# Performance work log

Measured on AMD Instinct MI355X. Metric: run time of the kernel, lower is better.

The kernel has to match this reference:

```python
import jax, jax.numpy as jnp
import numpy as np

N, M_CHE, M_VDW, B = 20000, 20, 20, 200
H, E, NODE_IN, NCONV = 128, 20, 13, 3
CHE_CUTOFF, VDW_CUTOFF = 8.0, 12.0


def setup_inputs() -> dict:
    key = jax.random.key(0)
    ks = jax.random.split(key, 16)
    s = 0.05
    inp = {}
    inp['atoms_embed'] = jax.random.normal(ks[0], (N, NODE_IN), jnp.float32)
    inp['che_nbrs_fea'] = jax.random.uniform(ks[1], (N, M_CHE), jnp.float32, 0.5, CHE_CUTOFF * 1.1)
    inp['vdw_nbrs_fea'] = jax.random.uniform(ks[2], (N, M_VDW), jnp.float32, 0.5, VDW_CUTOFF * 1.1)
    inp['che_nbrs_idx'] = jax.random.randint(ks[3], (N, M_CHE), 0, N)
    inp['vdw_nbrs_idx'] = jax.random.randint(ks[4], (N, M_VDW), 0, N)
    inp['num_atoms'] = jnp.full((B,), N // B, dtype=jnp.int32)  # 200 crystals x 100 atoms
    inp['emb_W'] = jax.random.normal(ks[5], (NODE_IN, H), jnp.float32) * s
    inp['emb_b'] = jnp.zeros((H,), jnp.float32)
    inp['che_filter_W'] = jax.random.normal(ks[6], (NCONV, E, H), jnp.float32) * s
    inp['che_filter_b'] = jnp.zeros((NCONV, H), jnp.float32)
    inp['che_fc_W'] = jax.random.normal(ks[7], (NCONV, 3 * H, 2 * H), jnp.float32) * s
    inp['che_fc_b'] = jnp.zeros((NCONV, 2 * H), jnp.float32)
    inp['vdw_filter_W'] = jax.random.normal(ks[8], (NCONV, E, H), jnp.float32) * s
    inp['vdw_filter_b'] = jnp.zeros((NCONV, H), jnp.float32)
    inp['vdw_fc_W'] = jax.random.normal(ks[9], (NCONV, 3 * H, 2 * H), jnp.float32) * s
    inp['vdw_fc_b'] = jnp.zeros((NCONV, 2 * H), jnp.float32)
    inp['fc1_W'] = jax.random.normal(ks[10], (H, H), jnp.float32) * s
    inp['fc1_b'] = jnp.zeros((H,), jnp.float32)
    inp['out_W'] = jax.random.normal(ks[11], (H, 1), jnp.float32) * s
    inp['out_b'] = jnp.zeros((1,), jnp.float32)
    return inp


def _rbf(d, cutoff):
    # sinc-like radial basis with cosine envelope; zero beyond cutoff
    k = jnp.arange(1, E + 1, dtype=d.dtype)  # [E]
    de = d[..., None]  # [N, M, 1]
    r = jnp.where(de < cutoff, jnp.sin(de * k * (jnp.pi / cutoff)) / de, jnp.zeros((), d.dtype))
    env = 0.5 * (jnp.cos(jnp.pi * d / cutoff) + 1.0)
    return r * env[..., None]  # [N, M, E]


def _conv_half(nodes, rbf_e, idx, fW, fb, gW, gb):
    n, m = idx.shape
    edges = rbf_e @ fW + fb  # [N, M, H]
    self_fea = jnp.broadcast_to(nodes[:, None, :], (n, m, nodes.shape[1]))
    total = jnp.concatenate([self_fea, edges, nodes[idx]], axis=2)  # [N, M, 3H]
    gated = total @ gW + gb  # [N, M, 2H]
    filt, core = jnp.split(gated, 2, axis=2)
    return jnp.sum(jax.nn.sigmoid(filt) * jax.nn.softplus(core), axis=1)  # [N, H]


def reference(atoms_embed, che_nbrs_fea, che_nbrs_idx, vdw_nbrs_fea, vdw_nbrs_idx,
              num_atoms, emb_W, emb_b, che_filter_W, che_filter_b, che_fc_W, che_fc_b,
              vdw_filter_W, vdw_filter_b, vdw_fc_W, vdw_fc_b, fc1_W, fc1_b, out_W, out_b):
    nodes = atoms_embed @ emb_W + emb_b  # [N, H]
    che_rbf = _rbf(che_nbrs_fea, CHE_CUTOFF)
    vdw_rbf = _rbf(vdw_nbrs_fea, VDW_CUTOFF)
    for i in range(NCONV):
        che = _conv_half(nodes, che_rbf, che_nbrs_idx, che_filter_W[i], che_filter_b[i], che_fc_W[i], che_fc_b[i])
        vdw = _conv_half(nodes, vdw_rbf, vdw_nbrs_idx, vdw_filter_W[i], vdw_filter_b[i], vdw_fc_W[i], vdw_fc_b[i])
        nodes = jax.nn.softplus(nodes + che + vdw)
    # per-crystal mean pooling from contiguous atom ranges given by num_atoms
    ends = jnp.cumsum(num_atoms)
    seg = jnp.searchsorted(ends, jnp.arange(nodes.shape[0]), side='right')
    sums = jax.ops.segment_sum(nodes, seg, num_segments=B)
    crys = sums / num_atoms[:, None].astype(nodes.dtype)  # [B, H]
    crys = jax.nn.softplus(jax.nn.softplus(crys) @ fc1_W + fc1_b)
    predict = (crys @ out_W + out_b)[:, 0]  # [B]
    return predict
```

## Files before the change

kernel.cpp:

```cpp
#include <hip/hip_runtime.h>
#include <hip/hip_bf16.h>
#include <math.h>

#define NN 20000
#define MM 20
#define EE 20
#define HH 128
#define BB 200
#define NCONV 3
#define CHE_CUT 8.0f
#define VDW_CUT 12.0f
#define PI_F 3.14159265358979323846f
#define LOG2E_F 1.44269504088896340736f
#define LN2_F 0.69314718055994530942f

typedef __fp16 half2_t __attribute__((ext_vector_type(2)));
typedef _Float16 f16x8 __attribute__((ext_vector_type(8)));
typedef float f32x4 __attribute__((ext_vector_type(4)));

__device__ __forceinline__ float exp2_(float x) {
#if __has_builtin(__builtin_amdgcn_exp2f)
    return __builtin_amdgcn_exp2f(x);
#else
    return exp2f(x);
#endif
}
__device__ __forceinline__ float log2_(float x) {
#if __has_builtin(__builtin_amdgcn_logf)
    return __builtin_amdgcn_logf(x);
#else
    return log2f(x);
#endif
}
__device__ __forceinline__ float rcp_(float x) {
#if __has_builtin(__builtin_amdgcn_rcpf)
    return __builtin_amdgcn_rcpf(x);
#else
    return 1.f / x;
#endif
}
__device__ __forceinline__ float sp_(float x) {
    return (x > 15.f) ? x : LN2_F * log2_(1.f + exp2_(x * LOG2E_F));
}
__device__ __forceinline__ float fdot2_(half2_t a, half2_t b, float c) {
#if __has_builtin(__builtin_amdgcn_fdot2)
    return __builtin_amdgcn_fdot2(a, b, c, false);
#else
    return (float)a.x * (float)b.x + (float)a.y * (float)b.y + c;
#endif
}

__global__ void prep_bias(const float* __restrict__ cfb, const float* __restrict__ cgW,
                          const float* __restrict__ cgb,
                          const float* __restrict__ vfb, const float* __restrict__ vgW,
                          const float* __restrict__ vgb, float* __restrict__ bc) {
    int half = blockIdx.y;
    int l = blockIdx.z;
    int j = threadIdx.x;
    const float* fb = half ? vfb : cfb;
    const float* gW = half ? vgW : cgW;
    const float* gb = half ? vgb : cgb;
    const float* gWe = gW + ((size_t)l * 384 + 128) * 256;
    const float* brow = fb + (size_t)l * HH;
    float acc = gb[(size_t)l * 256 + j];
    for (int k = 0; k < HH; ++k) acc = fmaf(brow[k], gWe[k * 256 + j], acc);
    bc[((size_t)l * 2 + half) * 256 + j] = acc * LOG2E_F;
}

__global__ void prep_bwc(const float* __restrict__ cfW, const float* __restrict__ cgW,
                         const float* __restrict__ vfW, const float* __restrict__ vgW,
                         _Float16* __restrict__ bwc) {
    int nt = blockIdx.x;
    int half = blockIdx.y;
    int l = blockIdx.z;
    int tid = threadIdx.x;
    int k = tid >> 4, nc = tid & 15;
    int t = (nt & 7) * 16 + nc;
    int gcol = (nt >> 3) * 128 + t;
    const float* fW = half ? vfW : cfW;
    const float* gW = half ? vgW : cgW;
    const float* gWe = gW + ((size_t)l * 384 + 128) * 256;
    float val = 0.f;
    if (k < EE) {
        const float* frow = fW + ((size_t)l * EE + k) * HH;
        for (int kk = 0; kk < HH; ++kk) val = fmaf(frow[kk], gWe[kk * 256 + gcol], val);
        val *= LOG2E_F;
    }
    bwc[(((size_t)(l * 2 + half) * 16 + nt) * 64 + (k >> 3) * 16 + nc) * 8 + (k & 7)] = (_Float16)val;
}

__global__ void prep_bpk(const float* __restrict__ cgW, const float* __restrict__ vgW,
                         _Float16* __restrict__ bpk) {
    int i = blockIdx.x * 256 + threadIdx.x;
    if (i >= NCONV * 128 * 1024) return;
    int l = i >> 17;
    int rem = i & 131071;
    int k = rem >> 10;
    int c = rem & 1023;
    int half = (c >> 8) & 1;
    const float* src = half ? vgW : cgW;
    int grow = l * 384 + ((c < 512) ? k : 256 + k);
    float val = src[(size_t)grow * 256 + (c & 255)] * LOG2E_F;
    int nt = c >> 4, nc = c & 15;
    int s = k >> 5, kq = (k >> 3) & 3, j = k & 7;
    bpk[(size_t)l * 131072 + (((size_t)nt * 4 + s) * 64 + kq * 16 + nc) * 8 + j] = (_Float16)val;
}

__global__ void embed_kernel(const float* __restrict__ atoms, const float* __restrict__ W,
                             const float* __restrict__ bias, float* __restrict__ nodes,
                             _Float16* __restrict__ nodes_h) {
    int n = blockIdx.x, t = threadIdx.x;
    const float* arow = atoms + (size_t)n * 13;
    float acc = bias[t];
    #pragma unroll
    for (int k = 0; k < 13; ++k) acc = fmaf(arow[k], W[k * HH + t], acc);
    nodes[(size_t)n * HH + t] = acc;
    nodes_h[(size_t)n * HH + t] = (_Float16)acc;
}

__global__ void rbf_kernel(const float* __restrict__ che_fea, const float* __restrict__ vdw_fea,
                           _Float16* __restrict__ rfrag) {
    int i = blockIdx.x * blockDim.x + threadIdx.x;
    if (i >= 2 * NN * MM) return;
    bool isv = i >= NN * MM;
    int rem = isv ? i - NN * MM : i;
    int n = rem / MM, m = rem % MM;
    float d = isv ? vdw_fea[rem] : che_fea[rem];
    float cutoff = isv ? VDW_CUT : CHE_CUT;
    float x = d * (PI_F / cutoff);
    float s1 = sinf(x), c1 = cosf(x);
    float env = 0.5f * (c1 + 1.f);
    float scale = (d < cutoff) ? (env / d) : 0.f;
    float out[EE];
    float skm1 = 0.f, sk = s1;
    #pragma unroll
    for (int e = 0; e < EE; ++e) {
        out[e] = sk * scale;
        float nx = 2.f * c1 * sk - skm1;
        skm1 = sk; sk = nx;
    }
    int mt = m >> 4, la = m & 15;
    _Float16* base = rfrag + (((size_t)(isv ? NN + n : n) * 2 + mt) * 64) * 8 + la * 8;
    f16x8 v0, v1, v2, v3;
    #pragma unroll
    for (int j = 0; j < 8; ++j) {
        v0[j] = (_Float16)out[j];
        v1[j] = (_Float16)out[8 + j];
        v2[j] = (j < 4) ? (_Float16)out[16 + j] : (_Float16)0.f;
        v3[j] = (_Float16)0.f;
    }
    *(f16x8*)(base) = v0;
    *(f16x8*)(base + 128) = v1;
    *(f16x8*)(base + 256) = v2;
    *(f16x8*)(base + 384) = v3;
}

__global__ __launch_bounds__(256)
void gemm_mfma(const _Float16* __restrict__ Ah, const _Float16* __restrict__ Bpk,
               half2_t* __restrict__ Spk, half2_t* __restrict__ Ypk) {
    int lane = threadIdx.x & 63;
    int wv = threadIdx.x >> 6;
    int m0 = blockIdx.x * 16;
    int la = lane & 15;
    int quad = lane >> 4;
    int k0 = quad * 8;

    f16x8 af[4];
    {
        const _Float16* arow = Ah + (size_t)(m0 + la) * 128 + k0;
        #pragma unroll
        for (int s = 0; s < 4; ++s)
            af[s] = *(const f16x8*)(arow + s * 32);
    }

    const f16x8* bp = (const f16x8*)Bpk;
    int ntf0 = wv * 16;
    half2_t* dst = (wv & 2) ? Ypk : Spk;
    int wbase = (wv & 1) * 128 + la;

    f16x8 fb[4], cb[4], nfb[4], ncb[4];
    #pragma unroll
    for (int s = 0; s < 4; ++s) {
        fb[s] = bp[((size_t)ntf0 * 4 + s) * 64 + lane];
        cb[s] = bp[((size_t)(ntf0 + 8) * 4 + s) * 64 + lane];
    }
    for (int p = 0; p < 8; ++p) {
        if (p < 7) {
            #pragma unroll
            for (int s = 0; s < 4; ++s) {
                nfb[s] = bp[((size_t)(ntf0 + p + 1) * 4 + s) * 64 + lane];
                ncb[s] = bp[((size_t)(ntf0 + 9 + p) * 4 + s) * 64 + lane];
            }
        }
        f32x4 accf = {0.f, 0.f, 0.f, 0.f};
        f32x4 accc = {0.f, 0.f, 0.f, 0.f};
        #pragma unroll
        for (int s = 0; s < 4; ++s) {
            accf = __builtin_amdgcn_mfma_f32_16x16x32_f16(af[s], fb[s], accf, 0, 0, 0);
            accc = __builtin_amdgcn_mfma_f32_16x16x32_f16(af[s], cb[s], accc, 0, 0, 0);
        }
        int row = m0 + quad * 4;
        int word = wbase + p * 16;
        #pragma unroll
        for (int i = 0; i < 4; ++i) {
            half2_t pk = __builtin_amdgcn_cvt_pkrtz(accf[i], accc[i]);
            dst[(size_t)(row + i) * 256 + word] = pk;
        }
        #pragma unroll
        for (int s = 0; s < 4; ++s) { fb[s] = nfb[s]; cb[s] = ncb[s]; }
    }
}

#define GSTRIDE 132
__global__ __launch_bounds__(128)
void edge_kernel(const float* __restrict__ nodes_in, float* __restrict__ nodes_out,
                 _Float16* __restrict__ nodes_h,
                 const half2_t* __restrict__ Spk, const half2_t* __restrict__ Ypk,
                 const _Float16* __restrict__ rfrag,
                 const int* __restrict__ idx_che, const int* __restrict__ idx_vdw,
                 const _Float16* __restrict__ bwc,
                 const float* __restrict__ bC) {
    __shared__ half2_t G2[40 * GSTRIDE];
    int t = threadIdx.x;
    int lane = t & 63;
    int wv = t >> 6;
    int n = blockIdx.x;

    const int* ic = idx_che + (size_t)n * MM;
    const int* iv = idx_vdw + (size_t)n * MM;
    int jc[MM], jv[MM];
    #pragma unroll
    for (int m = 0; m < MM; ++m) jc[m] = ic[m];
    #pragma unroll
    for (int m = 0; m < MM; ++m) jv[m] = iv[m];

    half2_t yw[2 * MM];
    #pragma unroll
    for (int m = 0; m < MM; ++m) yw[m] = Ypk[(size_t)jc[m] * 256 + t];
    #pragma unroll
    for (int m = 0; m < MM; ++m) yw[MM + m] = Ypk[(size_t)jv[m] * 256 + 128 + t];

    half2_t spc = Spk[(size_t)n * 256 + t];
    half2_t spv = Spk[(size_t)n * 256 + 128 + t];
    float old = nodes_in[(size_t)n * HH + t];
    float sCf = bC[t] + (float)spc.x;
    float sCc = bC[128 + t] + (float)spc.y;
    float sVf = bC[256 + t] + (float)spv.x;
    float sVc = bC[384 + t] + (float)spv.y;

    const half2_t ONE0 = {(__fp16)1.f, (__fp16)0.f};
    const half2_t ZERO1 = {(__fp16)0.f, (__fp16)1.f};
    int quad = lane >> 4;
    int cla = lane & 15;
    float acc = 0.f;

    #pragma unroll
    for (int h = 0; h < 2; ++h) {
        const _Float16* rf = rfrag + ((size_t)(h * NN + n) * 2) * 512;
        f16x8 a0 = *(const f16x8*)(rf + lane * 8);
        f16x8 a1 = *(const f16x8*)(rf + 512 + lane * 8);
        const f16x8* bw = (const f16x8*)bwc + ((size_t)h * 16) * 64;
        int rbase = h * 20;
        #pragma unroll
        for (int p = 0; p < 4; ++p) {
            int pg = wv * 4 + p;
            f16x8 bf = bw[(size_t)pg * 64 + lane];
            f16x8 bcfr = bw[(size_t)(8 + pg) * 64 + lane];
            f32x4 g0f = {0.f, 0.f, 0.f, 0.f};
            f32x4 g0c = {0.f, 0.f, 0.f, 0.f};
            f32x4 g1f = {0.f, 0.f, 0.f, 0.f};
            f32x4 g1c = {0.f, 0.f, 0.f, 0.f};
            g0f = __builtin_amdgcn_mfma_f32_16x16x32_f16(a0, bf, g0f, 0, 0, 0);
            g0c = __builtin_amdgcn_mfma_f32_16x16x32_f16(a0, bcfr, g0c, 0, 0, 0);
            g1f = __builtin_amdgcn_mfma_f32_16x16x32_f16(a1, bf, g1f, 0, 0, 0);
            g1c = __builtin_amdgcn_mfma_f32_16x16x32_f16(a1, bcfr, g1c, 0, 0, 0);
            int base = pg * 16 + cla;
            #pragma unroll
            for (int i = 0; i < 4; ++i)
                G2[(rbase + quad * 4 + i) * GSTRIDE + base] = __builtin_amdgcn_cvt_pkrtz(g0f[i], g0c[i]);
            if (quad == 0) {
                #pragma unroll
                for (int i = 0; i < 4; ++i)
                    G2[(rbase + 16 + i) * GSTRIDE + base] = __builtin_amdgcn_cvt_pkrtz(g1f[i], g1c[i]);
            }
        }
    }
    __syncthreads();

    #pragma unroll
    for (int m = 0; m < MM; ++m) {
        half2_t g = G2[m * GSTRIDE + t];
        half2_t w = yw[m];
        float gf = fdot2_(g, ONE0, fdot2_(w, ONE0, sCf));
        float gc = fdot2_(g, ZERO1, fdot2_(w, ZERO1, sCc));
        float uu = rcp_(1.f + exp2_(-gf));
        float p = log2_(1.f + exp2_(gc));
        p = (gc > 24.f) ? gc : p;
        acc = fmaf(p, uu, acc);
    }
    #pragma unroll
    for (int m = 0; m < MM; ++m) {
        half2_t g = G2[(20 + m) * GSTRIDE + t];
        half2_t w = yw[MM + m];
        float gf = fdot2_(g, ONE0, fdot2_(w, ONE0, sVf));
        float gc = fdot2_(g, ZERO1, fdot2_(w, ZERO1, sVc));
        float uu = rcp_(1.f + exp2_(-gf));
        float p = log2_(1.f + exp2_(gc));
        p = (gc > 24.f) ? gc : p;
        acc = fmaf(p, uu, acc);
    }
    float res = sp_(fmaf(acc, LN2_F, old));
    nodes_out[(size_t)n * HH + t] = res;
    nodes_h[(size_t)n * HH + t] = (_Float16)res;
}

__global__ void pool_kernel(const float* __restrict__ nodes, const int* __restrict__ num_atoms,
                            const float* __restrict__ fc1_W, const float* __restrict__ fc1_b,
                            const float* __restrict__ out_W, const float* __restrict__ out_b,
                            float* __restrict__ out) {
    __shared__ float sh[HH];
    __shared__ float red[HH];
    int b = blockIdx.x, t = threadIdx.x;
    int start = 0;
    for (int i = 0; i < b; ++i) start += num_atoms[i];
    int cnt = num_atoms[b];
    float sum = 0.f;
    for (int a = 0; a < cnt; ++a) sum += nodes[(size_t)(start + a) * HH + t];
    float mean = sum / (float)cnt;
    sh[t] = sp_(mean);
    __syncthreads();
    float o = fc1_b[t];
    #pragma unroll 4
    for (int k = 0; k < HH; ++k) o = fmaf(sh[k], fc1_W[k * HH + t], o);
    red[t] = sp_(o) * out_W[t];
    __syncthreads();
    if (t == 0) {
        float tot = 0.f;
        for (int k = 0; k < HH; ++k) tot += red[k];
        out[b] = tot + out_b[0];
    }
}

extern "C" void kernel_launch(void* const* d_in, const int* in_sizes, int n_in,
                              void* d_out, int out_size, void* d_ws, size_t ws_size,
                              hipStream_t stream) {
    const float* atoms_embed   = (const float*)d_in[0];
    const float* che_nbrs_fea  = (const float*)d_in[1];
    const float* vdw_nbrs_fea  = (const float*)d_in[2];
    const int*   che_nbrs_idx  = (const int*)  d_in[3];
    const int*   vdw_nbrs_idx  = (const int*)  d_in[4];
    const int*   num_atoms     = (const int*)  d_in[5];
    const float* emb_W         = (const float*)d_in[6];
    const float* emb_b         = (const float*)d_in[7];
    const float* che_filter_W  = (const float*)d_in[8];
    const float* che_filter_b  = (const float*)d_in[9];
    const float* che_fc_W      = (const float*)d_in[10];
    const float* che_fc_b      = (const float*)d_in[11];
    const float* vdw_filter_W  = (const float*)d_in[12];
    const float* vdw_filter_b  = (const float*)d_in[13];
    const float* vdw_fc_W      = (const float*)d_in[14];
    const float* vdw_fc_b      = (const float*)d_in[15];
    const float* fc1_W         = (const float*)d_in[16];
    const float* fc1_b         = (const float*)d_in[17];
    const float* out_W         = (const float*)d_in[18];
    const float* out_b         = (const float*)d_in[19];
    float* out = (float*)d_out;

    float* w = (float*)d_ws;
    float* nodesA   = w;
    float* nodesB   = nodesA + (size_t)NN * HH;
    _Float16* nodes_h = (_Float16*)(nodesB + (size_t)NN * HH);
    half2_t* Spk    = (half2_t*)(nodes_h + (size_t)NN * HH);
    half2_t* Ypk    = Spk + (size_t)NN * 256;
    _Float16* rfrag = (_Float16*)(Ypk + (size_t)NN * 256);
    _Float16* bpk   = rfrag + (size_t)2 * NN * 2 * 512;
    _Float16* bwc   = bpk + (size_t)NCONV * 131072;
    float* bc       = (float*)(bwc + (size_t)NCONV * 2 * 16 * 512);

    hipMemsetAsync(rfrag, 0, (size_t)2 * NN * 2 * 512 * sizeof(_Float16), stream);

    prep_bias<<<dim3(1, 2, NCONV), 256, 0, stream>>>(
        che_filter_b, che_fc_W, che_fc_b, vdw_filter_b, vdw_fc_W, vdw_fc_b, bc);
    prep_bwc<<<dim3(16, 2, NCONV), 512, 0, stream>>>(
        che_filter_W, che_fc_W, vdw_filter_W, vdw_fc_W, bwc);
    prep_bpk<<<(NCONV * 128 * 1024 + 255) / 256, 256, 0, stream>>>(che_fc_W, vdw_fc_W, bpk);
    embed_kernel<<<NN, HH, 0, stream>>>(atoms_embed, emb_W, emb_b, nodesA, nodes_h);
    rbf_kernel<<<(2 * NN * MM + 255) / 256, 256, 0, stream>>>(che_nbrs_fea, vdw_nbrs_fea, rfrag);

    float* cur = nodesA;
    float* nxt = nodesB;
    for (int l = 0; l < NCONV; ++l) {
        gemm_mfma<<<NN / 16, 256, 0, stream>>>(nodes_h, bpk + (size_t)l * 131072, Spk, Ypk);
        edge_kernel<<<NN, HH, 0, stream>>>(
            cur, nxt, nodes_h, Spk, Ypk, rfrag, che_nbrs_idx, vdw_nbrs_idx,
            bwc + (size_t)l * 2 * 16 * 512, bc + (size_t)l * 512);
        float* tmp = cur; cur = nxt; nxt = tmp;
    }

    pool_kernel<<<BB, HH, 0, stream>>>(cur, num_atoms, fc1_W, fc1_b, out_W, out_b, out);
}
```

Measured before the change: 523.7 us.

## Split che and vdw halves of edge kernel across two thread groups

The edge kernel now launches 256 threads per atom instead of 128. Threads 0-127 handle the chemical neighbors and threads 128-255 the van der Waals neighbors, each wave pair computing its own MFMA filter tile, and the two partial sums are combined through shared memory before the softplus. This halves per-thread serial work and register pressure (20 instead of 40 gathered values) to raise parallelism and latency hiding. In exchange it adds a second barrier and a shared-memory reduction, leaves half the threads idle at the end, and adds the gathered and self terms in packed fp16 before the dot, which slightly changes rounding.

```diff
diff --git a/kernel.cpp b/kernel.cpp
--- a/kernel.cpp
+++ b/kernel.cpp
@@ -212,7 +212,7 @@
 }
 
 #define GSTRIDE 132
-__global__ __launch_bounds__(128)
+__global__ __launch_bounds__(256)
 void edge_kernel(const float* __restrict__ nodes_in, float* __restrict__ nodes_out,
                  _Float16* __restrict__ nodes_h,
                  const half2_t* __restrict__ Spk, const half2_t* __restrict__ Ypk,
@@ -221,49 +221,43 @@
                  const _Float16* __restrict__ bwc,
                  const float* __restrict__ bC) {
     __shared__ half2_t G2[40 * GSTRIDE];
+    __shared__ float red[HH];
     int t = threadIdx.x;
     int lane = t & 63;
     int wv = t >> 6;
     int n = blockIdx.x;
-
-    const int* ic = idx_che + (size_t)n * MM;
-    const int* iv = idx_vdw + (size_t)n * MM;
-    int jc[MM], jv[MM];
-    #pragma unroll
-    for (int m = 0; m < MM; ++m) jc[m] = ic[m];
-    #pragma unroll
-    for (int m = 0; m < MM; ++m) jv[m] = iv[m];
-
-    half2_t yw[2 * MM];
-    #pragma unroll
-    for (int m = 0; m < MM; ++m) yw[m] = Ypk[(size_t)jc[m] * 256 + t];
-    #pragma unroll
-    for (int m = 0; m < MM; ++m) yw[MM + m] = Ypk[(size_t)jv[m] * 256 + 128 + t];
-
-    half2_t spc = Spk[(size_t)n * 256 + t];
-    half2_t spv = Spk[(size_t)n * 256 + 128 + t];
-    float old = nodes_in[(size_t)n * HH + t];
-    float sCf = bC[t] + (float)spc.x;
-    float sCc = bC[128 + t] + (float)spc.y;
-    float sVf = bC[256 + t] + (float)spv.x;
-    float sVc = bC[384 + t] + (float)spv.y;
+    int h2 = t >> 7;
+    int tc = t & 127;
+
+    const int* idxp = h2 ? (idx_vdw + (size_t)n * MM) : (idx_che + (size_t)n * MM);
+    int jx[MM];
+    #pragma unroll
+    for (int m = 0; m < MM; ++m) jx[m] = idxp[m];
+
+    half2_t yw[MM];
+    #pragma unroll
+    for (int m = 0; m < MM; ++m) yw[m] = Ypk[(size_t)jx[m] * 256 + h2 * 128 + tc];
+
+    half2_t spx = Spk[(size_t)n * 256 + h2 * 128 + tc];
+    float old = (h2 == 0) ? nodes_in[(size_t)n * HH + tc] : 0.f;
+    float sf = bC[h2 * 256 + tc] + (float)spx.x;
+    float sc = bC[h2 * 256 + 128 + tc] + (float)spx.y;
 
     const half2_t ONE0 = {(__fp16)1.f, (__fp16)0.f};
     const half2_t ZERO1 = {(__fp16)0.f, (__fp16)1.f};
     int quad = lane >> 4;
     int cla = lane & 15;
-    float acc = 0.f;
-
-    #pragma unroll
-    for (int h = 0; h < 2; ++h) {
-        const _Float16* rf = rfrag + ((size_t)(h * NN + n) * 2) * 512;
+
+    {
+        int hw = wv >> 1;
+        int rbase = hw * 20;
+        const _Float16* rf = rfrag + ((size_t)(hw * NN + n) * 2) * 512;
         f16x8 a0 = *(const f16x8*)(rf + lane * 8);
         f16x8 a1 = *(const f16x8*)(rf + 512 + lane * 8);
-        const f16x8* bw = (const f16x8*)bwc + ((size_t)h * 16) * 64;
-        int rbase = h * 20;
+        const f16x8* bw = (const f16x8*)bwc + ((size_t)hw * 16) * 64;
         #pragma unroll
         for (int p = 0; p < 4; ++p) {
-            int pg = wv * 4 + p;
+            int pg = (wv & 1) * 4 + p;
             f16x8 bf = bw[(size_t)pg * 64 + lane];
             f16x8 bcfr = bw[(size_t)(8 + pg) * 64 + lane];
             f32x4 g0f = {0.f, 0.f, 0.f, 0.f};
@@ -287,31 +281,26 @@
     }
     __syncthreads();
 
+    float acc = 0.f;
+    int grow = h2 * 20;
     #pragma unroll
     for (int m = 0; m < MM; ++m) {
-        half2_t g = G2[m * GSTRIDE + t];
-        half2_t w = yw[m];
-        float gf = fdot2_(g, ONE0, fdot2_(w, ONE0, sCf));
-        float gc = fdot2_(g, ZERO1, fdot2_(w, ZERO1, sCc));
+        half2_t g = G2[(grow + m) * GSTRIDE + tc];
+        half2_t gw = g + yw[m];
+        float gf = fdot2_(gw, ONE0, sf);
+        float gc = fdot2_(gw, ZERO1, sc);
         float uu = rcp_(1.f + exp2_(-gf));
         float p = log2_(1.f + exp2_(gc));
         p = (gc > 24.f) ? gc : p;
         acc = fmaf(p, uu, acc);
     }
-    #pragma unroll
-    for (int m = 0; m < MM; ++m) {
-        half2_t g = G2[(20 + m) * GSTRIDE + t];
-        half2_t w = yw[MM + m];
-        float gf = fdot2_(g, ONE0, fdot2_(w, ONE0, sVf));
-        float gc = fdot2_(g, ZERO1, fdot2_(w, ZERO1, sVc));
-        float uu = rcp_(1.f + exp2_(-gf));
-        float p = log2_(1.f + exp2_(gc));
-        p = (gc > 24.f) ? gc : p;
-        acc = fmaf(p, uu, acc);
-    }
-    float res = sp_(fmaf(acc, LN2_F, old));
-    nodes_out[(size_t)n * HH + t] = res;
-    nodes_h[(size_t)n * HH + t] = (_Float16)res;
+    if (h2) red[tc] = acc;
+    __syncthreads();
+    if (!h2) {
+        float res = sp_(fmaf(acc + red[tc], LN2_F, old));
+        nodes_out[(size_t)n * HH + tc] = res;
+        nodes_h[(size_t)n * HH + tc] = (_Float16)res;
+    }
 }
 
 __global__ void pool_kernel(const float* __restrict__ nodes, const int* __restrict__ num_atoms,
@@ -391,7 +380,7 @@
     float* nxt = nodesB;
     for (int l = 0; l < NCONV; ++l) {
         gemm_mfma<<<NN / 16, 256, 0, stream>>>(nodes_h, bpk + (size_t)l * 131072, Spk, Ypk);
-        edge_kernel<<<NN, HH, 0, stream>>>(
+        edge_kernel<<<NN, 256, 0, stream>>>(
             cur, nxt, nodes_h, Spk, Ypk, rfrag, che_nbrs_idx, vdw_nbrs_idx,
             bwc + (size_t)l * 2 * 16 * 512, bc + (size_t)l * 512);
         float* tmp = cur; cur = nxt; nxt = tmp;
```

Result: faster. 498.3 us (-4.8%).
